# Performance work log

Hardware: AMD Instinct MI355X
Metric: run time of the kernel (lower is better)

## Reference

```python
import jax, jax.numpy as jnp
from jax import lax
import numpy as np

B, T, V, E, H = 64, 256, 50000, 256, 512
HD = H // 2            # per-direction hidden
TAGS, START, STOP = 20, 18, 19


def setup_inputs() -> dict:
    key = jax.random.key(0)
    ks = jax.random.split(key, 18)
    s = 0.1  # param scale
    sentences = jax.random.randint(ks[0], (B, T), 0, V)
    emb = jax.random.normal(ks[1], (V, E), jnp.float32) * s
    Wih_f = jax.random.normal(ks[2], (4 * HD, E), jnp.float32) * s
    Whh_f = jax.random.normal(ks[3], (4 * HD, HD), jnp.float32) * s
    bih_f = jax.random.normal(ks[4], (4 * HD,), jnp.float32) * s
    bhh_f = jax.random.normal(ks[5], (4 * HD,), jnp.float32) * s
    Wih_b = jax.random.normal(ks[6], (4 * HD, E), jnp.float32) * s
    Whh_b = jax.random.normal(ks[7], (4 * HD, HD), jnp.float32) * s
    bih_b = jax.random.normal(ks[8], (4 * HD,), jnp.float32) * s
    bhh_b = jax.random.normal(ks[9], (4 * HD,), jnp.float32) * s
    Wl = jax.random.normal(ks[10], (TAGS, H), jnp.float32) * s
    bl = jax.random.normal(ks[11], (TAGS,), jnp.float32) * s
    trans = jax.random.normal(ks[12], (TAGS, TAGS), jnp.float32)
    trans = trans.at[:, START].set(-1000.0).at[STOP, :].set(-1000.0)
    # init_hidden(): uniform(-1, 1), shape [2*num_layer, B, HD] for h and c
    h0 = jax.random.uniform(ks[13], (2, B, HD), jnp.float32, -1.0, 1.0)
    c0 = jax.random.uniform(ks[14], (2, B, HD), jnp.float32, -1.0, 1.0)
    return dict(sentences=sentences, emb=emb, Wih_f=Wih_f, Whh_f=Whh_f,
                bih_f=bih_f, bhh_f=bhh_f, Wih_b=Wih_b, Whh_b=Whh_b,
                bih_b=bih_b, bhh_b=bhh_b, Wl=Wl, bl=bl, trans=trans,
                h0=h0, c0=c0)


def _lstm_dir(x_tbe, Wih, Whh, bih, bhh, h, c):
    # x_tbe: [T,B,E]; PyTorch gate order i,f,g,o
    gx = jnp.einsum('tbe,ge->tbg', x_tbe, Wih) + bih + bhh  # [T,B,4HD]
    def step(carry, gx_t):
        h, c = carry
        g = gx_t + h @ Whh.T
        i, f, gg, o = jnp.split(g, 4, axis=-1)
        c = jax.nn.sigmoid(f) * c + jax.nn.sigmoid(i) * jnp.tanh(gg)
        h = jax.nn.sigmoid(o) * jnp.tanh(c)
        return (h, c), h
    _, hs = lax.scan(step, (h, c), gx)
    return hs  # [T,B,HD]


def reference(sentences, emb, Wih_f, Whh_f, bih_f, bhh_f,
              Wih_b, Whh_b, bih_b, bhh_b, Wl, bl, trans, h0, c0):
    x = emb[sentences].transpose(1, 0, 2)             # [T,B,E]
    hf = _lstm_dir(x, Wih_f, Whh_f, bih_f, bhh_f, h0[0], c0[0])
    hb = _lstm_dir(x[::-1], Wih_b, Whh_b, bih_b, bhh_b, h0[1], c0[1])[::-1]
    out = jnp.concatenate([hf, hb], axis=-1)          # [T,B,H]
    logits = out @ Wl.T + bl                          # [T,B,TAGS]

    # Viterbi DP (all sentences at full length T, vectorized over batch)
    trellis0 = logits[0]                              # [B,TAGS]
    def vstep(prev, logit_t):
        v = prev[:, :, None] + trans[None]            # [B, prev_tag, cur_tag]
        new = logit_t + v.max(axis=1)
        return new, (new, v.argmax(axis=1))
    _, (trellis_rest, bps) = lax.scan(vstep, trellis0, logits[1:])
    trellis = jnp.concatenate([trellis0[None], trellis_rest], 0)  # [T,B,TAGS]

    last_tag = jnp.argmax(trellis[-1], axis=-1)       # [B]
    def bstep(tag, bp):                               # bp: [B,TAGS]
        prev = jnp.take_along_axis(bp, tag[:, None], axis=1)[:, 0]
        return prev, prev
    _, path_rev = lax.scan(bstep, last_tag, bps[::-1])
    path = jnp.concatenate([path_rev[::-1], last_tag[None]], 0)  # [T,B]

    probs = jnp.take_along_axis(jax.nn.softmax(trellis, axis=-1),
                                path[:, :, None], axis=2)[:, :, 0]  # [T,B]
    scores = trellis[-1].max(axis=-1)                 # [B]
    return scores, path.T, probs.T
```

## Files before the change

kernel.cpp:

```cpp
#include <hip/hip_runtime.h>

typedef unsigned int uint;
typedef unsigned short ushort;
typedef __attribute__((ext_vector_type(4))) float f4;
typedef __attribute__((ext_vector_type(8))) short bf8;

#define T_ 256
#define B_ 64
#define E_ 256
#define HD_ 256
#define NTAG 20

#define GX_OFF 0ull
#define LG_OFF 33554432ull
#define FLG_OFF 33882112ull
#define Q_OFFF 33884160ull

#define WHHF_HI 0u
#define WHHB_HI 524288u
#define WIHF_HI 1048576u
#define WIHB_HI 1572864u
#define LO_D    262144u
#define WL_HI   2097152u
#define WL_LO   2107392u
#define HS_HI   2117632u
#define HS_LO   10539008u
#define HS_DIR  4210688ull

#define ECTL_CNT 512u
#define ECTL_LDR 520u

__device__ __forceinline__ ushort f2bf(float x){
  uint u = __float_as_uint(x);
  uint r = (u + 0x7fffu + ((u >> 16) & 1u)) >> 16;
  return (ushort)r;
}
__device__ __forceinline__ float bf2f(ushort h){ return __uint_as_float(((uint)h) << 16); }
__device__ __forceinline__ void splitf(float x, ushort &h, ushort &l){
  h = f2bf(x);
  l = f2bf(x - bf2f(h));
}
__device__ __forceinline__ f4 mfma16(bf8 a, bf8 b, f4 c){
  return __builtin_amdgcn_mfma_f32_16x16x32_bf16(a, b, c, 0, 0, 0);
}
__device__ __forceinline__ float sigm(float x){ return 1.0f / (1.0f + expf(-x)); }

#define LDH(dst, base, off) \
  asm volatile("global_load_dwordx4 %0, %1, off offset:" #off " sc0" \
               : "=v"(dst) : "v"(base))
#define LDG16(dst, base, off) \
  asm volatile("global_load_dwordx4 %0, %1, off offset:" #off \
               : "=v"(dst) : "v"(base))
#define ST2(base, off, val) \
  asm volatile("global_store_short %0, %1, off offset:" #off " sc0" \
               :: "v"(base), "v"(val) : "memory")
#define STFLAG(p, v) \
  asm volatile("global_store_dword %0, %1, off sc0" :: "v"(p), "v"(v) : "memory")

__global__ void k0_split(const float* __restrict__ whhF, const float* __restrict__ whhB,
                         const float* __restrict__ wihF, const float* __restrict__ wihB,
                         const float* __restrict__ wl, const float* __restrict__ h0,
                         ushort* __restrict__ q, uint* __restrict__ flags){
  uint stride = gridDim.x * blockDim.x;
  for (uint i = blockIdx.x * blockDim.x + threadIdx.x; i < 1093632u; i += stride){
    float x; uint hbase;
    if (i < 262144u){ x = whhF[i]; hbase = WHHF_HI + i; }
    else if (i < 524288u){ x = whhB[i - 262144u]; hbase = WHHB_HI + (i - 262144u); }
    else if (i < 786432u){ x = wihF[i - 524288u]; hbase = WIHF_HI + (i - 524288u); }
    else if (i < 1048576u){ x = wihB[i - 786432u]; hbase = WIHB_HI + (i - 786432u); }
    else if (i < 1058816u){
      uint j = i - 1048576u;
      ushort h, l; splitf(wl[j], h, l);
      q[WL_HI + j] = h; q[WL_LO + j] = l;
      continue;
    } else if (i < 1091584u){
      uint j = i - 1058816u;
      uint dir = j >> 14, rem = j & 16383u;
      ushort h, l; splitf(h0[j], h, l);
      q[HS_HI + dir * (uint)HS_DIR + rem] = h;
      q[HS_LO + dir * (uint)HS_DIR + rem] = l;
      continue;
    } else {
      uint j = i - 1091584u;
      __hip_atomic_store(&flags[j], (j == ECTL_LDR) ? 0xffffffffu : 0u,
                         __ATOMIC_RELAXED, __HIP_MEMORY_SCOPE_AGENT);
      continue;
    }
    ushort h, l; splitf(x, h, l);
    q[hbase] = h; q[hbase + LO_D] = l;
  }
}

__global__ __launch_bounds__(256) void k1_gx(const int* __restrict__ sents,
    const float* __restrict__ emb, const ushort* __restrict__ q,
    const float* __restrict__ bihF, const float* __restrict__ bhhF,
    const float* __restrict__ bihB, const float* __restrict__ bhhB,
    float* __restrict__ gx)
{
  __shared__ ushort Bs[2][64][256];
  const int tid = threadIdx.x;
  const int dir = blockIdx.z;
  const int n0 = blockIdx.x * 64;
  const int r0 = blockIdx.y * 64;
  const ushort* whi = q + (dir ? WIHB_HI : WIHF_HI);

  for (int cid = tid; cid < 4096; cid += 256){
    int half = cid >> 11;
    int c = (cid >> 5) & 63;
    int kc = cid & 31;
    const ushort* src = whi + half * LO_D + (size_t)(n0 + c) * 256 + kc * 8;
    uint4 v = *(const uint4*)src;
    *(uint4*)&Bs[half][c][(kc ^ (c & 31)) * 8] = v;
  }
  __syncthreads();

  const int w = tid >> 6, l = tid & 63;
  const int lrow = l & 15, lk8 = (l >> 4) * 8;
  const int r = r0 + w * 16 + lrow;
  const int t = r >> 6, b = r & 63;
  const int tok = sents[b * T_ + (dir ? (T_ - 1 - t) : t)];
  const float* arow = emb + (size_t)tok * E_;

  f4 acc[4];
  #pragma unroll
  for (int i = 0; i < 4; i++){ acc[i][0]=0.f; acc[i][1]=0.f; acc[i][2]=0.f; acc[i][3]=0.f; }

  for (int ks = 0; ks < 8; ks++){
    const float* ap = arow + ks * 32 + lk8;
    f4 v0 = *(const f4*)ap;
    f4 v1 = *(const f4*)(ap + 4);
    bf8 ah, al;
    #pragma unroll
    for (int j = 0; j < 4; j++){
      ushort hh, ll;
      splitf(v0[j], hh, ll); ah[j] = (short)hh; al[j] = (short)ll;
      splitf(v1[j], hh, ll); ah[4 + j] = (short)hh; al[4 + j] = (short)ll;
    }
    const int kc = ks * 4 + (l >> 4);
    #pragma unroll
    for (int nt = 0; nt < 4; nt++){
      const int c = nt * 16 + lrow;
      const int skc = kc ^ (c & 31);
      bf8 bh = *(const bf8*)&Bs[0][c][skc * 8];
      bf8 blo = *(const bf8*)&Bs[1][c][skc * 8];
      acc[nt] = mfma16(ah, bh, acc[nt]);
      acc[nt] = mfma16(ah, blo, acc[nt]);
      acc[nt] = mfma16(al, bh, acc[nt]);
    }
  }

  const float* bih = dir ? bihB : bihF;
  const float* bhh = dir ? bhhB : bhhF;
  #pragma unroll
  for (int nt = 0; nt < 4; nt++){
    int col = n0 + nt * 16 + lrow;
    float bias = bih[col] + bhh[col];
    int gate = col >> 8, ug = (col >> 4) & 15;
    #pragma unroll
    for (int reg = 0; reg < 4; reg++){
      int row = r0 + w * 16 + (l >> 4) * 4 + reg;
      int tt = row >> 6, b2 = row & 63;
      int ctid = ((b2 >> 4) << 6) | (((b2 >> 2) & 3) << 4) | lrow;
      gx[(((size_t)(dir * 16 + ug) * 256 + tt) * 256 + ctid) * 16
         + (b2 & 3) * 4 + gate] = acc[nt][reg] + bias;
    }
  }
}


#define K2_STEP(TT, GC)                                                             \
{                                                                                   \
  const int t_ = (TT);                                                              \
  asm volatile("s_waitcnt vmcnt(4)" ::: "memory");                                  \
  __builtin_amdgcn_sched_barrier(0);                                                \
  f4 acc[4];                                                                        \
  _Pragma("unroll")                                                                 \
  for (int i = 0; i < 4; i++){ acc[i][0]=0.f; acc[i][1]=0.f; acc[i][2]=0.f; acc[i][3]=0.f; } \
  _Pragma("unroll")                                                                 \
  for (int ks = 0; ks < 8; ks++){                                                   \
    const int kc = ks * 4 + (l >> 4);                                               \
    _Pragma("unroll")                                                               \
    for (int nt = 0; nt < 4; nt++){                                                 \
      const int c = nt * 16 + lrow;                                                 \
      const int skc = kc ^ (c & 31);                                                \
      bf8 bh  = *(const bf8*)&Bs[0][c][skc * 8];                                    \
      bf8 blo = *(const bf8*)&Bs[1][c][skc * 8];                                    \
      acc[nt] = mfma16(ah[ks], bh, acc[nt]);                                        \
      acc[nt] = mfma16(ah[ks], blo, acc[nt]);                                       \
      acc[nt] = mfma16(al[ks], bh, acc[nt]);                                        \
    }                                                                               \
  }                                                                                 \
  {                                                                                 \
    ushort* oHi = hHiD + (size_t)(t_ + 1) * 16384 + erow * 256 + unit;              \
    ushort* oLo = hLoD + (size_t)(t_ + 1) * 16384 + erow * 256 + unit;              \
    ushort hh_[4], ll_[4];                                                          \
    _Pragma("unroll")                                                               \
    for (int reg = 0; reg < 4; reg++){                                              \
      float g0 = acc[0][reg] + GC[reg][0];                                          \
      float g1 = acc[1][reg] + GC[reg][1];                                          \
      float g2 = acc[2][reg] + GC[reg][2];                                          \
      float g3 = acc[3][reg] + GC[reg][3];                                          \
      float cn = sigm(g1) * creg[reg] + sigm(g0) * tanhf(g2);                       \
      float hn = sigm(g3) * tanhf(cn);                                              \
      creg[reg] = cn;                                                               \
      splitf(hn, hh_[reg], ll_[reg]);                                               \
    }                                                                               \
    ST2(oHi, 0, hh_[0]);    ST2(oLo, 0, ll_[0]);                                    \
    ST2(oHi, 512, hh_[1]);  ST2(oLo, 512, ll_[1]);                                  \
    ST2(oHi, 1024, hh_[2]); ST2(oLo, 1024, ll_[2]);                                 \
    ST2(oHi, 1536, hh_[3]); ST2(oLo, 1536, ll_[3]);                                 \
  }                                                                                 \
  if (t_ + 1 < T_){                                                                 \
    asm volatile("s_waitcnt vmcnt(0)" ::: "memory");                                \
    __builtin_amdgcn_sched_barrier(0);                                              \
    __syncthreads();                                                                \
    uint e = (uint)(t_ + 1);                                                        \
    if (tid == 0) STFLAG(fb + (ub << 4), e);                                        \
    if (w == 0){                                                                    \
      uint fv = 0xffffffffu;                                                        \
      const uint* fp = fb + ((l & 15) << 4);                                        \
      int guard = 0;                                                                \
      do {                                                                          \
        if (l < 16) asm volatile("global_load_dword %0, %1, off sc0"                \
                                 : "=v"(fv) : "v"(fp));                             \
        asm volatile("s_waitcnt vmcnt(0)" ::: "memory");                            \
      } while (!__all(fv >= e) && ++guard < 16384);                                 \
    }                                                                               \
    __syncthreads();                                                                \
    __builtin_amdgcn_sched_barrier(0);                                              \
    const ushort* rh = hHiD + (size_t)(t_ + 1) * 16384 + arow * 256 + lk8;          \
    const ushort* rl = hLoD + (size_t)(t_ + 1) * 16384 + arow * 256 + lk8;          \
    LDH(ah[0], rh, 0);   LDH(ah[1], rh, 64);  LDH(ah[2], rh, 128); LDH(ah[3], rh, 192); \
    LDH(ah[4], rh, 256); LDH(ah[5], rh, 320); LDH(ah[6], rh, 384); LDH(ah[7], rh, 448); \
    LDH(al[0], rl, 0);   LDH(al[1], rl, 64);  LDH(al[2], rl, 128); LDH(al[3], rl, 192); \
    LDH(al[4], rl, 256); LDH(al[5], rl, 320); LDH(al[6], rl, 384); LDH(al[7], rl, 448); \
    int t2 = (t_ + 2 < T_) ? (t_ + 2) : (T_ - 1);                                   \
    const float* pn = gxp + ((size_t)t2 * 256 + tid) * 16;                          \
    LDG16(GC[0], pn, 0); LDG16(GC[1], pn, 16);                                      \
    LDG16(GC[2], pn, 32); LDG16(GC[3], pn, 48);                                     \
  }                                                                                 \
}

__global__ __launch_bounds__(256, 1) void k2_persist(const ushort* __restrict__ q,
    const float* __restrict__ gx, const float* __restrict__ c0,
    ushort* __restrict__ hsHi, ushort* __restrict__ hsLo, uint* __restrict__ flags)
{
  __shared__ ushort Bs[2][64][256];
  __shared__ int s_tk;
  const int tid = threadIdx.x;

  if (tid == 0){
    uint xcc;
    asm volatile("s_getreg_b32 %0, hwreg(HW_REG_XCC_ID)" : "=s"(xcc));
    xcc &= 7u;
    uint my = atomicAdd(&flags[ECTL_CNT + xcc], 1u);
    if (my == 31u) atomicCAS(&flags[ECTL_LDR], 0xffffffffu, xcc);
    uint L = 0xffffffffu;
    for (int g = 0; g < (1 << 20); ++g){
      L = __hip_atomic_load(&flags[ECTL_LDR], __ATOMIC_RELAXED,
                            __HIP_MEMORY_SCOPE_AGENT);
      if (L != 0xffffffffu) break;
    }
    s_tk = (L == xcc && my < 32u) ? (int)my : -1;
  }
  __syncthreads();
  const int ticket = s_tk;
  if (ticket < 0) return;

  const int dir = ticket >> 4;
  const int ub  = ticket & 15;
  const int u0  = ub * 16;
  const ushort* whi = q + (dir ? WHHB_HI : WHHF_HI);

  for (int cid = tid; cid < 4096; cid += 256){
    int half = cid >> 11;
    int c = (cid >> 5) & 63;
    int kc = cid & 31;
    int grow = (c >> 4) * 256 + u0 + (c & 15);
    const ushort* src = whi + half * LO_D + (size_t)grow * 256 + kc * 8;
    uint4 v = *(const uint4*)src;
    *(uint4*)&Bs[half][c][(kc ^ (c & 31)) * 8] = v;
  }
  __syncthreads();

  const int w = tid >> 6, l = tid & 63;
  const int lrow = l & 15, lk8 = (l >> 4) * 8;
  const int arow = w * 16 + lrow;
  const int unit = u0 + lrow;
  const int erow = w * 16 + (l >> 4) * 4;

  float creg[4];
  #pragma unroll
  for (int reg = 0; reg < 4; reg++)
    creg[reg] = c0[dir * 16384 + (erow + reg) * 256 + unit];
  asm volatile("" :: "v"(creg[0]), "v"(creg[1]), "v"(creg[2]), "v"(creg[3]));

  ushort* hHiD = hsHi + (size_t)dir * HS_DIR;
  ushort* hLoD = hsLo + (size_t)dir * HS_DIR;
  const float* gxp = gx + (size_t)(dir * 16 + ub) * 1048576ull;
  uint* fb = flags + dir * 1024;

  f4 ga[4], gb[4];
  bf8 ah[8], al[8];

  {
    const float* p0 = gxp + (size_t)tid * 16;
    LDG16(ga[0], p0, 0); LDG16(ga[1], p0, 16); LDG16(ga[2], p0, 32); LDG16(ga[3], p0, 48);
    const ushort* rh = hHiD + arow * 256 + lk8;
    const ushort* rl = hLoD + arow * 256 + lk8;
    LDH(ah[0], rh, 0);   LDH(ah[1], rh, 64);  LDH(ah[2], rh, 128); LDH(ah[3], rh, 192);
    LDH(ah[4], rh, 256); LDH(ah[5], rh, 320); LDH(ah[6], rh, 384); LDH(ah[7], rh, 448);
    LDH(al[0], rl, 0);   LDH(al[1], rl, 64);  LDH(al[2], rl, 128); LDH(al[3], rl, 192);
    LDH(al[4], rl, 256); LDH(al[5], rl, 320); LDH(al[6], rl, 384); LDH(al[7], rl, 448);
    const float* p1 = gxp + ((size_t)256 + tid) * 16;
    LDG16(gb[0], p1, 0); LDG16(gb[1], p1, 16); LDG16(gb[2], p1, 32); LDG16(gb[3], p1, 48);
  }

  #pragma unroll 1
  for (int t = 0; t < T_; t += 2){
    K2_STEP(t, ga);
    K2_STEP(t + 1, gb);
  }
  asm volatile("s_waitcnt vmcnt(0)" ::: "memory");
}

__global__ __launch_bounds__(256) void k3_logits(const ushort* __restrict__ q,
    const float* __restrict__ bl, float* __restrict__ logits)
{
  __shared__ ushort Bs[2][32][512];
  const int tid = threadIdx.x;
  const int r0 = blockIdx.x * 64;
  const ushort* hsHi = q + HS_HI;
  const ushort* hsLo = q + HS_LO;

  for (int cid = tid; cid < 4096; cid += 256){
    int half = cid >> 11;
    int c = (cid >> 6) & 31;
    int kc = cid & 63;
    uint4 v; v.x = 0; v.y = 0; v.z = 0; v.w = 0;
    if (c < NTAG){
      const ushort* src = q + (half ? WL_LO : WL_HI) + (size_t)c * 512 + kc * 8;
      v = *(const uint4*)src;
    }
    *(uint4*)&Bs[half][c][(kc ^ (c & 31)) * 8] = v;
  }
  __syncthreads();

  const int w = tid >> 6, l = tid & 63;
  const int lrow = l & 15, lk8 = (l >> 4) * 8;
  const int r = r0 + w * 16 + lrow;
  const int t = r >> 6, b = r & 63;

  f4 acc[2];
  #pragma unroll
  for (int i = 0; i < 2; i++){ acc[i][0]=0.f; acc[i][1]=0.f; acc[i][2]=0.f; acc[i][3]=0.f; }

  for (int ks = 0; ks < 16; ks++){
    int k = ks * 32 + lk8;
    size_t off;
    if (k < 256)
      off = (size_t)(t + 1) * 16384 + (size_t)b * 256 + k;
    else
      off = HS_DIR + (size_t)(256 - t) * 16384 + (size_t)b * 256 + (k - 256);
    bf8 ah = *(const bf8*)&hsHi[off];
    bf8 al = *(const bf8*)&hsLo[off];
    int kc = k >> 3;
    #pragma unroll
    for (int nt = 0; nt < 2; nt++){
      int c = nt * 16 + lrow;
      int skc = kc ^ (c & 31);
      bf8 bh  = *(const bf8*)&Bs[0][c][skc * 8];
      bf8 blo = *(const bf8*)&Bs[1][c][skc * 8];
      acc[nt] = mfma16(ah, bh, acc[nt]);
      acc[nt] = mfma16(ah, blo, acc[nt]);
      acc[nt] = mfma16(al, bh, acc[nt]);
    }
  }

  #pragma unroll
  for (int nt = 0; nt < 2; nt++){
    int tag = nt * 16 + lrow;
    if (tag < NTAG){
      float bias = bl[tag];
      #pragma unroll
      for (int reg = 0; reg < 4; reg++){
        int row = r0 + w * 16 + (l >> 4) * 4 + reg;
        logits[(size_t)row * NTAG + tag] = acc[nt][reg] + bias;
      }
    }
  }
}

__global__ __launch_bounds__(64) void k4_viterbi(const float* __restrict__ logits,
    const float* __restrict__ trans, float* __restrict__ out)
{
  const int b = blockIdx.x, tid = threadIdx.x;
  __shared__ float tr[NTAG][NTAG];
  __shared__ float trell[T_][NTAG];
  __shared__ unsigned char bp[T_][NTAG];
  __shared__ int path[T_];
  __shared__ float cur[NTAG], nv[NTAG];

  for (int i = tid; i < NTAG * NTAG; i += 64) tr[i / NTAG][i % NTAG] = trans[i];
  if (tid < NTAG){
    float v = logits[(size_t)b * NTAG + tid];
    cur[tid] = v; trell[0][tid] = v;
  }
  __syncthreads();

  for (int t = 1; t < T_; t++){
    if (tid < NTAG){
      float best = -3.0e38f; int bi = 0;
      #pragma unroll
      for (int p = 0; p < NTAG; p++){
        float v = cur[p] + tr[p][tid];
        if (v > best){ best = v; bi = p; }
      }
      float nvv = logits[((size_t)t * 64 + b) * NTAG + tid] + best;
      nv[tid] = nvv; trell[t][tid] = nvv; bp[t][tid] = (unsigned char)bi;
    }
    __syncthreads();
    if (tid < NTAG) cur[tid] = nv[tid];
    __syncthreads();
  }

  if (tid == 0){
    float best = -3.0e38f; int bi = 0;
    for (int c = 0; c < NTAG; c++){
      if (trell[T_ - 1][c] > best){ best = trell[T_ - 1][c]; bi = c; }
    }
    out[b] = best;
    path[T_ - 1] = bi;
    for (int t = T_ - 1; t >= 1; t--) path[t - 1] = bp[t][path[t]];
  }
  __syncthreads();

  for (int t = tid; t < T_; t += 64){
    float m = -3.0e38f;
    for (int c = 0; c < NTAG; c++) m = fmaxf(m, trell[t][c]);
    float s = 0.f;
    for (int c = 0; c < NTAG; c++) s += expf(trell[t][c] - m);
    float p = expf(trell[t][path[t]] - m) / s;
    out[64 + (size_t)b * T_ + t] = (float)path[t];
    out[64 + 64 * T_ + (size_t)b * T_ + t] = p;
  }
}

extern "C" void kernel_launch(void* const* d_in, const int* in_sizes, int n_in,
                              void* d_out, int out_size, void* d_ws, size_t ws_size,
                              hipStream_t stream){
  (void)in_sizes; (void)n_in; (void)out_size; (void)ws_size;
  const int*   sents = (const int*)d_in[0];
  const float* emb   = (const float*)d_in[1];
  const float* wihF  = (const float*)d_in[2];
  const float* whhF  = (const float*)d_in[3];
  const float* bihF  = (const float*)d_in[4];
  const float* bhhF  = (const float*)d_in[5];
  const float* wihB  = (const float*)d_in[6];
  const float* whhB  = (const float*)d_in[7];
  const float* bihB  = (const float*)d_in[8];
  const float* bhhB  = (const float*)d_in[9];
  const float* wl    = (const float*)d_in[10];
  const float* bl    = (const float*)d_in[11];
  const float* trans = (const float*)d_in[12];
  const float* h0    = (const float*)d_in[13];
  const float* c0    = (const float*)d_in[14];

  float* wsf    = (float*)d_ws;
  ushort* q     = (ushort*)(wsf + Q_OFFF);
  float* gx     = wsf + GX_OFF;
  float* logits = wsf + LG_OFF;
  uint* flags   = (uint*)(wsf + FLG_OFF);
  float* out    = (float*)d_out;
  ushort* hsHi  = q + HS_HI;
  ushort* hsLo  = q + HS_LO;

  k0_split<<<1024, 256, 0, stream>>>(whhF, whhB, wihF, wihB, wl, h0, q, flags);
  k1_gx<<<dim3(16, 256, 2), 256, 0, stream>>>(sents, emb, q, bihF, bhhF, bihB, bhhB, gx);

  {
    const ushort* qa = q; const float* gxa = gx; const float* c0a = c0;
    ushort* hia = hsHi; ushort* loa = hsLo; uint* fla = flags;
    void* args[] = { (void*)&qa, (void*)&gxa, (void*)&c0a,
                     (void*)&hia, (void*)&loa, (void*)&fla };
    hipLaunchCooperativeKernel((const void*)k2_persist, dim3(256), dim3(256),
                               args, 0, stream);
  }

  k3_logits<<<256, 256, 0, stream>>>(q, bl, logits);
  k4_viterbi<<<64, 64, 0, stream>>>(logits, trans, out);
}
```

Before: 1.588 ms.

## Switch LSTM matmuls to three-way bf16 split and fuse weight splitting into kernels

Moves the recurrent and input-projection GEMMs from a two-term bf16 hi/lo split to a three-term hi/mid/lo split with six MFMAs per tile. This doubles the MFMA work in the serial recurrence and adds a third hidden-state load stream. Weight splitting now happens inside k1 and k2 from the fp32 weights, dropping the separate pre-split pass and its global traffic. k1 tiles shrink to 32 columns to fit the third LDS plane, the low hidden part goes into a ping-pong buffer, and k2 moves from a cooperative launch to a normal launch. The added work on the critical path means the main aim looks like accuracy rather than speed.

Result: slower. 2.225 ms (+40.1%).

```diff
diff --git a/kernel.cpp b/kernel.cpp
--- a/kernel.cpp
+++ b/kernel.cpp
@@ -16,16 +16,13 @@
 #define FLG_OFF 33882112ull
 #define Q_OFFF 33884160ull
 
-#define WHHF_HI 0u
-#define WHHB_HI 524288u
-#define WIHF_HI 1048576u
-#define WIHB_HI 1572864u
-#define LO_D    262144u
-#define WL_HI   2097152u
-#define WL_LO   2107392u
-#define HS_HI   2117632u
-#define HS_LO   10539008u
-#define HS_DIR  4210688ull
+#define WL_HI 0u
+#define WL_LO 10240u
+#define HS_HI 20480u
+#define HS_MID 8441856u
+#define HS_LOPP 16863232u
+#define HS_DIR 4210688ull
+#define LOPP_DIR 32768u
 
 #define ECTL_CNT 512u
 #define ECTL_LDR 520u
@@ -39,6 +36,12 @@
 __device__ __forceinline__ void splitf(float x, ushort &h, ushort &l){
   h = f2bf(x);
   l = f2bf(x - bf2f(h));
+}
+__device__ __forceinline__ void splitf3(float x, ushort &h, ushort &m, ushort &l){
+  h = f2bf(x);
+  float r1 = x - bf2f(h);
+  m = f2bf(r1);
+  l = f2bf(r1 - bf2f(m));
 }
 __device__ __forceinline__ f4 mfma16(bf8 a, bf8 b, f4 c){
   return __builtin_amdgcn_mfma_f32_16x16x32_bf16(a, b, c, 0, 0, 0);
@@ -57,60 +60,48 @@
 #define STFLAG(p, v) \
   asm volatile("global_store_dword %0, %1, off sc0" :: "v"(p), "v"(v) : "memory")
 
-__global__ void k0_split(const float* __restrict__ whhF, const float* __restrict__ whhB,
-                         const float* __restrict__ wihF, const float* __restrict__ wihB,
-                         const float* __restrict__ wl, const float* __restrict__ h0,
+__global__ void k0_split(const float* __restrict__ wl, const float* __restrict__ h0,
                          ushort* __restrict__ q, uint* __restrict__ flags){
   uint stride = gridDim.x * blockDim.x;
-  for (uint i = blockIdx.x * blockDim.x + threadIdx.x; i < 1093632u; i += stride){
-    float x; uint hbase;
-    if (i < 262144u){ x = whhF[i]; hbase = WHHF_HI + i; }
-    else if (i < 524288u){ x = whhB[i - 262144u]; hbase = WHHB_HI + (i - 262144u); }
-    else if (i < 786432u){ x = wihF[i - 524288u]; hbase = WIHF_HI + (i - 524288u); }
-    else if (i < 1048576u){ x = wihB[i - 786432u]; hbase = WIHB_HI + (i - 786432u); }
-    else if (i < 1058816u){
-      uint j = i - 1048576u;
-      ushort h, l; splitf(wl[j], h, l);
-      q[WL_HI + j] = h; q[WL_LO + j] = l;
-      continue;
-    } else if (i < 1091584u){
-      uint j = i - 1058816u;
+  for (uint i = blockIdx.x * blockDim.x + threadIdx.x; i < 45056u; i += stride){
+    if (i < 10240u){
+      ushort h, l; splitf(wl[i], h, l);
+      q[WL_HI + i] = h; q[WL_LO + i] = l;
+    } else if (i < 43008u){
+      uint j = i - 10240u;
       uint dir = j >> 14, rem = j & 16383u;
-      ushort h, l; splitf(h0[j], h, l);
+      ushort h, m, l; splitf3(h0[j], h, m, l);
       q[HS_HI + dir * (uint)HS_DIR + rem] = h;
-      q[HS_LO + dir * (uint)HS_DIR + rem] = l;
-      continue;
+      q[HS_MID + dir * (uint)HS_DIR + rem] = m;
+      q[HS_LOPP + dir * LOPP_DIR + rem] = l;
     } else {
-      uint j = i - 1091584u;
+      uint j = i - 43008u;
       __hip_atomic_store(&flags[j], (j == ECTL_LDR) ? 0xffffffffu : 0u,
                          __ATOMIC_RELAXED, __HIP_MEMORY_SCOPE_AGENT);
-      continue;
-    }
-    ushort h, l; splitf(x, h, l);
-    q[hbase] = h; q[hbase + LO_D] = l;
+    }
   }
 }
 
 __global__ __launch_bounds__(256) void k1_gx(const int* __restrict__ sents,
-    const float* __restrict__ emb, const ushort* __restrict__ q,
+    const float* __restrict__ emb, const float* __restrict__ wihF,
+    const float* __restrict__ wihB,
     const float* __restrict__ bihF, const float* __restrict__ bhhF,
     const float* __restrict__ bihB, const float* __restrict__ bhhB,
     float* __restrict__ gx)
 {
-  __shared__ ushort Bs[2][64][256];
+  __shared__ ushort Bs[3][32][256];
   const int tid = threadIdx.x;
   const int dir = blockIdx.z;
-  const int n0 = blockIdx.x * 64;
+  const int n0 = blockIdx.x * 32;
   const int r0 = blockIdx.y * 64;
-  const ushort* whi = q + (dir ? WIHB_HI : WIHF_HI);
-
-  for (int cid = tid; cid < 4096; cid += 256){
-    int half = cid >> 11;
-    int c = (cid >> 5) & 63;
-    int kc = cid & 31;
-    const ushort* src = whi + half * LO_D + (size_t)(n0 + c) * 256 + kc * 8;
-    uint4 v = *(const uint4*)src;
-    *(uint4*)&Bs[half][c][(kc ^ (c & 31)) * 8] = v;
+  const float* wih = dir ? wihB : wihF;
+
+  for (int v = tid; v < 8192; v += 256){
+    int c = v >> 8, k = v & 255;
+    float x = wih[(size_t)(n0 + c) * 256 + k];
+    ushort h, m, l; splitf3(x, h, m, l);
+    int pos = (((k >> 3) ^ (c & 31)) << 3) + (k & 7);
+    Bs[0][c][pos] = h; Bs[1][c][pos] = m; Bs[2][c][pos] = l;
   }
   __syncthreads();
 
@@ -121,30 +112,36 @@
   const int tok = sents[b * T_ + (dir ? (T_ - 1 - t) : t)];
   const float* arow = emb + (size_t)tok * E_;
 
-  f4 acc[4];
+  f4 acc[2];
   #pragma unroll
-  for (int i = 0; i < 4; i++){ acc[i][0]=0.f; acc[i][1]=0.f; acc[i][2]=0.f; acc[i][3]=0.f; }
+  for (int i = 0; i < 2; i++){ acc[i][0]=0.f; acc[i][1]=0.f; acc[i][2]=0.f; acc[i][3]=0.f; }
 
   for (int ks = 0; ks < 8; ks++){
     const float* ap = arow + ks * 32 + lk8;
     f4 v0 = *(const f4*)ap;
     f4 v1 = *(const f4*)(ap + 4);
-    bf8 ah, al;
+    bf8 ah, am, al;
     #pragma unroll
     for (int j = 0; j < 4; j++){
-      ushort hh, ll;
-      splitf(v0[j], hh, ll); ah[j] = (short)hh; al[j] = (short)ll;
-      splitf(v1[j], hh, ll); ah[4 + j] = (short)hh; al[4 + j] = (short)ll;
+      ushort hh, mm, ll;
+      splitf3(v0[j], hh, mm, ll);
+      ah[j] = (short)hh; am[j] = (short)mm; al[j] = (short)ll;
+      splitf3(v1[j], hh, mm, ll);
+      ah[4 + j] = (short)hh; am[4 + j] = (short)mm; al[4 + j] = (short)ll;
     }
     const int kc = ks * 4 + (l >> 4);
     #pragma unroll
-    for (int nt = 0; nt < 4; nt++){
+    for (int nt = 0; nt < 2; nt++){
       const int c = nt * 16 + lrow;
       const int skc = kc ^ (c & 31);
       bf8 bh = *(const bf8*)&Bs[0][c][skc * 8];
-      bf8 blo = *(const bf8*)&Bs[1][c][skc * 8];
+      bf8 bm = *(const bf8*)&Bs[1][c][skc * 8];
+      bf8 bl = *(const bf8*)&Bs[2][c][skc * 8];
       acc[nt] = mfma16(ah, bh, acc[nt]);
-      acc[nt] = mfma16(ah, blo, acc[nt]);
+      acc[nt] = mfma16(ah, bm, acc[nt]);
+      acc[nt] = mfma16(am, bh, acc[nt]);
+      acc[nt] = mfma16(ah, bl, acc[nt]);
+      acc[nt] = mfma16(am, bm, acc[nt]);
       acc[nt] = mfma16(al, bh, acc[nt]);
     }
   }
@@ -152,7 +149,7 @@
   const float* bih = dir ? bihB : bihF;
   const float* bhh = dir ? bhhB : bhhF;
   #pragma unroll
-  for (int nt = 0; nt < 4; nt++){
+  for (int nt = 0; nt < 2; nt++){
     int col = n0 + nt * 16 + lrow;
     float bias = bih[col] + bhh[col];
     int gate = col >> 8, ug = (col >> 4) & 15;
@@ -183,17 +180,22 @@
     for (int nt = 0; nt < 4; nt++){                                                 \
       const int c = nt * 16 + lrow;                                                 \
       const int skc = kc ^ (c & 31);                                                \
-      bf8 bh  = *(const bf8*)&Bs[0][c][skc * 8];                                    \
-      bf8 blo = *(const bf8*)&Bs[1][c][skc * 8];                                    \
+      bf8 bh = *(const bf8*)&Bs[0][c][skc * 8];                                     \
+      bf8 bm = *(const bf8*)&Bs[1][c][skc * 8];                                     \
+      bf8 bl = *(const bf8*)&Bs[2][c][skc * 8];                                     \
       acc[nt] = mfma16(ah[ks], bh, acc[nt]);                                        \
-      acc[nt] = mfma16(ah[ks], blo, acc[nt]);                                       \
+      acc[nt] = mfma16(ah[ks], bm, acc[nt]);                                        \
+      acc[nt] = mfma16(am[ks], bh, acc[nt]);                                        \
+      acc[nt] = mfma16(ah[ks], bl, acc[nt]);                                        \
+      acc[nt] = mfma16(am[ks], bm, acc[nt]);                                        \
       acc[nt] = mfma16(al[ks], bh, acc[nt]);                                        \
     }                                                                               \
   }                                                                                 \
   {                                                                                 \
     ushort* oHi = hHiD + (size_t)(t_ + 1) * 16384 + erow * 256 + unit;              \
-    ushort* oLo = hLoD + (size_t)(t_ + 1) * 16384 + erow * 256 + unit;              \
-    ushort hh_[4], ll_[4];                                                          \
+    ushort* oMd = hMidD + (size_t)(t_ + 1) * 16384 + erow * 256 + unit;             \
+    ushort* oLo = hLoPPD + (size_t)((t_ + 1) & 1) * 16384 + erow * 256 + unit;      \
+    ushort hh_[4], mm_[4], ll_[4];                                                  \
     _Pragma("unroll")                                                               \
     for (int reg = 0; reg < 4; reg++){                                              \
       float g0 = acc[0][reg] + GC[reg][0];                                          \
@@ -203,15 +205,15 @@
       float cn = sigm(g1) * creg[reg] + sigm(g0) * tanhf(g2);                       \
       float hn = sigm(g3) * tanhf(cn);                                              \
       creg[reg] = cn;                                                               \
-      splitf(hn, hh_[reg], ll_[reg]);                                               \
+      splitf3(hn, hh_[reg], mm_[reg], ll_[reg]);                                    \
     }                                                                               \
-    ST2(oHi, 0, hh_[0]);    ST2(oLo, 0, ll_[0]);                                    \
-    ST2(oHi, 512, hh_[1]);  ST2(oLo, 512, ll_[1]);                                  \
-    ST2(oHi, 1024, hh_[2]); ST2(oLo, 1024, ll_[2]);                                 \
-    ST2(oHi, 1536, hh_[3]); ST2(oLo, 1536, ll_[3]);                                 \
+    ST2(oHi, 0, hh_[0]);    ST2(oMd, 0, mm_[0]);    ST2(oLo, 0, ll_[0]);            \
+    ST2(oHi, 512, hh_[1]);  ST2(oMd, 512, mm_[1]);  ST2(oLo, 512, ll_[1]);          \
+    ST2(oHi, 1024, hh_[2]); ST2(oMd, 1024, mm_[2]); ST2(oLo, 1024, ll_[2]);         \
+    ST2(oHi, 1536, hh_[3]); ST2(oMd, 1536, mm_[3]); ST2(oLo, 1536, ll_[3]);         \
   }                                                                                 \
   if (t_ + 1 < T_){                                                                 \
-    asm volatile("s_waitcnt vmcnt(0)" ::: "memory");                                \
+    asm volatile("s_waitcnt vmcnt(0)" ::: "memory");        \
     __builtin_amdgcn_sched_barrier(0);                                              \
     __syncthreads();                                                                \
     uint e = (uint)(t_ + 1);                                                        \
@@ -229,9 +231,12 @@
     __syncthreads();                                                                \
     __builtin_amdgcn_sched_barrier(0);                                              \
     const ushort* rh = hHiD + (size_t)(t_ + 1) * 16384 + arow * 256 + lk8;          \
-    const ushort* rl = hLoD + (size_t)(t_ + 1) * 16384 + arow * 256 + lk8;          \
+    const ushort* rm = hMidD + (size_t)(t_ + 1) * 16384 + arow * 256 + lk8;         \
+    const ushort* rl = hLoPPD + (size_t)((t_ + 1) & 1) * 16384 + arow * 256 + lk8;  \
     LDH(ah[0], rh, 0);   LDH(ah[1], rh, 64);  LDH(ah[2], rh, 128); LDH(ah[3], rh, 192); \
     LDH(ah[4], rh, 256); LDH(ah[5], rh, 320); LDH(ah[6], rh, 384); LDH(ah[7], rh, 448); \
+    LDH(am[0], rm, 0);   LDH(am[1], rm, 64);  LDH(am[2], rm, 128); LDH(am[3], rm, 192); \
+    LDH(am[4], rm, 256); LDH(am[5], rm, 320); LDH(am[6], rm, 384); LDH(am[7], rm, 448); \
     LDH(al[0], rl, 0);   LDH(al[1], rl, 64);  LDH(al[2], rl, 128); LDH(al[3], rl, 192); \
     LDH(al[4], rl, 256); LDH(al[5], rl, 320); LDH(al[6], rl, 384); LDH(al[7], rl, 448); \
     int t2 = (t_ + 2 < T_) ? (t_ + 2) : (T_ - 1);                                   \
@@ -241,11 +246,12 @@
   }                                                                                 \
 }
 
-__global__ __launch_bounds__(256, 1) void k2_persist(const ushort* __restrict__ q,
+__global__ __launch_bounds__(256, 1) void k2_persist(
+    const float* __restrict__ whhF, const float* __restrict__ whhB,
     const float* __restrict__ gx, const float* __restrict__ c0,
-    ushort* __restrict__ hsHi, ushort* __restrict__ hsLo, uint* __restrict__ flags)
+    ushort* __restrict__ q, uint* __restrict__ flags)
 {
-  __shared__ ushort Bs[2][64][256];
+  __shared__ ushort Bs[3][64][256];
   __shared__ int s_tk;
   const int tid = threadIdx.x;
 
@@ -270,16 +276,16 @@
   const int dir = ticket >> 4;
   const int ub  = ticket & 15;
   const int u0  = ub * 16;
-  const ushort* whi = q + (dir ? WHHB_HI : WHHF_HI);
-
-  for (int cid = tid; cid < 4096; cid += 256){
-    int half = cid >> 11;
-    int c = (cid >> 5) & 63;
-    int kc = cid & 31;
+  uint* fb = flags + dir * 1024;
+  const float* whh = dir ? whhB : whhF;
+
+  for (int v = tid; v < 16384; v += 256){
+    int c = v >> 8, k = v & 255;
     int grow = (c >> 4) * 256 + u0 + (c & 15);
-    const ushort* src = whi + half * LO_D + (size_t)grow * 256 + kc * 8;
-    uint4 v = *(const uint4*)src;
-    *(uint4*)&Bs[half][c][(kc ^ (c & 31)) * 8] = v;
+    float x = whh[(size_t)grow * 256 + k];
+    ushort h, m, l; splitf3(x, h, m, l);
+    int pos = (((k >> 3) ^ (c & 31)) << 3) + (k & 7);
+    Bs[0][c][pos] = h; Bs[1][c][pos] = m; Bs[2][c][pos] = l;
   }
   __syncthreads();
 
@@ -295,21 +301,24 @@
     creg[reg] = c0[dir * 16384 + (erow + reg) * 256 + unit];
   asm volatile("" :: "v"(creg[0]), "v"(creg[1]), "v"(creg[2]), "v"(creg[3]));
 
-  ushort* hHiD = hsHi + (size_t)dir * HS_DIR;
-  ushort* hLoD = hsLo + (size_t)dir * HS_DIR;
+  ushort* hHiD   = q + HS_HI  + (size_t)dir * HS_DIR;
+  ushort* hMidD  = q + HS_MID + (size_t)dir * HS_DIR;
+  ushort* hLoPPD = q + HS_LOPP + dir * LOPP_DIR;
   const float* gxp = gx + (size_t)(dir * 16 + ub) * 1048576ull;
-  uint* fb = flags + dir * 1024;
 
   f4 ga[4], gb[4];
-  bf8 ah[8], al[8];
+  bf8 ah[8], am[8], al[8];
 
   {
     const float* p0 = gxp + (size_t)tid * 16;
     LDG16(ga[0], p0, 0); LDG16(ga[1], p0, 16); LDG16(ga[2], p0, 32); LDG16(ga[3], p0, 48);
     const ushort* rh = hHiD + arow * 256 + lk8;
-    const ushort* rl = hLoD + arow * 256 + lk8;
+    const ushort* rm = hMidD + arow * 256 + lk8;
+    const ushort* rl = hLoPPD + arow * 256 + lk8;
     LDH(ah[0], rh, 0);   LDH(ah[1], rh, 64);  LDH(ah[2], rh, 128); LDH(ah[3], rh, 192);
     LDH(ah[4], rh, 256); LDH(ah[5], rh, 320); LDH(ah[6], rh, 384); LDH(ah[7], rh, 448);
+    LDH(am[0], rm, 0);   LDH(am[1], rm, 64);  LDH(am[2], rm, 128); LDH(am[3], rm, 192);
+    LDH(am[4], rm, 256); LDH(am[5], rm, 320); LDH(am[6], rm, 384); LDH(am[7], rm, 448);
     LDH(al[0], rl, 0);   LDH(al[1], rl, 64);  LDH(al[2], rl, 128); LDH(al[3], rl, 192);
     LDH(al[4], rl, 256); LDH(al[5], rl, 320); LDH(al[6], rl, 384); LDH(al[7], rl, 448);
     const float* p1 = gxp + ((size_t)256 + tid) * 16;
@@ -331,7 +340,7 @@
   const int tid = threadIdx.x;
   const int r0 = blockIdx.x * 64;
   const ushort* hsHi = q + HS_HI;
-  const ushort* hsLo = q + HS_LO;
+  const ushort* hsMd = q + HS_MID;
 
   for (int cid = tid; cid < 4096; cid += 256){
     int half = cid >> 11;
@@ -363,7 +372,7 @@
     else
       off = HS_DIR + (size_t)(256 - t) * 16384 + (size_t)b * 256 + (k - 256);
     bf8 ah = *(const bf8*)&hsHi[off];
-    bf8 al = *(const bf8*)&hsLo[off];
+    bf8 al = *(const bf8*)&hsMd[off];
     int kc = k >> 3;
     #pragma unroll
     for (int nt = 0; nt < 2; nt++){
@@ -472,21 +481,11 @@
   float* logits = wsf + LG_OFF;
   uint* flags   = (uint*)(wsf + FLG_OFF);
   float* out    = (float*)d_out;
-  ushort* hsHi  = q + HS_HI;
-  ushort* hsLo  = q + HS_LO;
-
-  k0_split<<<1024, 256, 0, stream>>>(whhF, whhB, wihF, wihB, wl, h0, q, flags);
-  k1_gx<<<dim3(16, 256, 2), 256, 0, stream>>>(sents, emb, q, bihF, bhhF, bihB, bhhB, gx);
-
-  {
-    const ushort* qa = q; const float* gxa = gx; const float* c0a = c0;
-    ushort* hia = hsHi; ushort* loa = hsLo; uint* fla = flags;
-    void* args[] = { (void*)&qa, (void*)&gxa, (void*)&c0a,
-                     (void*)&hia, (void*)&loa, (void*)&fla };
-    hipLaunchCooperativeKernel((const void*)k2_persist, dim3(256), dim3(256),
-                               args, 0, stream);
-  }
-
+
+  k0_split<<<176, 256, 0, stream>>>(wl, h0, q, flags);
+  k1_gx<<<dim3(32, 256, 2), 256, 0, stream>>>(sents, emb, wihF, wihB,
+                                              bihF, bhhF, bihB, bhhB, gx);
+  k2_persist<<<256, 256, 0, stream>>>(whhF, whhB, gx, c0, q, flags);
   k3_logits<<<256, 256, 0, stream>>>(q, bl, logits);
   k4_viterbi<<<64, 64, 0, stream>>>(logits, trans, out);
 }
```
